# Kernel tuning notes

Measured on AMD Instinct MI355X. Metric: run time of the kernel, lower is better.

The kernel has to match this reference:

```python
import jax, jax.numpy as jnp
import numpy as np

B, NORB, N_UP, N_DN, HIDDEN = 1024, 128, 32, 32, 4096


def setup_inputs() -> dict:
    rng = np.random.default_rng(0)
    # Build valid occupancy configs: exactly N_UP up-electrons (bit 0) and
    # N_DN down-electrons (bit 1) per sample. Encoding: 0=empty,1=up,2=dn,3=updn.
    up_order = np.argsort(rng.random((B, NORB)), axis=1)
    dn_order = np.argsort(rng.random((B, NORB)), axis=1)
    up_bit = np.zeros((B, NORB), np.int32)
    dn_bit = np.zeros((B, NORB), np.int32)
    np.put_along_axis(up_bit, up_order[:, :N_UP], 1, axis=1)
    np.put_along_axis(dn_bit, dn_order[:, :N_DN], 1, axis=1)
    x = jnp.asarray(up_bit + 2 * dn_bit, dtype=jnp.int32)

    key = jax.random.key(0)
    k1, k2, k3 = jax.random.split(key, 3)
    orbitals = jax.random.normal(k1, (NORB, N_UP), jnp.float32)
    W1 = jax.random.normal(k2, (4 * NORB, HIDDEN), jnp.float32) / np.sqrt(4 * NORB)
    b1 = jnp.zeros((HIDDEN,), jnp.float32)
    W2 = jax.random.normal(k3, (HIDDEN, NORB * N_UP), jnp.float32) / np.sqrt(HIDDEN)
    b2 = jnp.zeros((NORB * N_UP,), jnp.float32)
    return {"x": x, "orbitals": orbitals, "W1": W1, "b1": b1, "W2": W2, "b2": b2}


def _occupancies_to_electrons(x, n_up, n_dn):
    # Per-spin sorted positions of occupied orbitals. Stable argsort on the
    # inverted mask keeps occupied sites first, in ascending orbital order.
    up_mask = (x & 1) == 1
    dn_mask = (x & 2) == 2
    y_up = jnp.argsort(jnp.where(up_mask, 0, 1), axis=-1, stable=True)[:, :n_up]
    y_dn = jnp.argsort(jnp.where(dn_mask, 0, 1), axis=-1, stable=True)[:, :n_dn]
    return y_up, y_dn


def reference(x, orbitals, W1, b1, W2, b2):
    Bsz, norb = x.shape
    n_up = orbitals.shape[1]

    # correction_fun: MLP on one-hot config -> [B, norb, n_up]
    h = jax.nn.one_hot(x, 4, dtype=W1.dtype).reshape(Bsz, -1)  # [B, 4*norb]
    h = jax.nn.relu(h @ W1 + b1)                               # [B, hidden]
    corrections = (h @ W2 + b2).reshape(Bsz, norb, n_up)       # [B, norb, n_up]

    y_up, y_dn = _occupancies_to_electrons(x, n_up, n_up)
    y_up = y_up[..., None]  # [B, n_up, 1]
    y_dn = y_dn[..., None]

    # gather orbital rows + correction rows per electron (spin-symmetric orbitals)
    phi_up = jnp.take_along_axis(orbitals[None], y_up, axis=1)  # [B, n_up, n_up]
    phi_dn = jnp.take_along_axis(orbitals[None], y_dn, axis=1)
    d_up = jnp.take_along_axis(corrections, y_up, axis=1)
    d_dn = jnp.take_along_axis(corrections, y_dn, axis=1)

    s_up, log_det_up = jnp.linalg.slogdet(phi_up + d_up)
    s_dn, log_det_dn = jnp.linalg.slogdet(phi_dn + d_dn)
    return log_det_up + log_det_dn + jnp.log(s_up * s_dn + 0j)  # complex [B]
```

## Files before the change

### kernel.cpp

```cpp
#include <hip/hip_runtime.h>
#include <cmath>

#define B_SZ  1024
#define NORB  128
#define NUP   32
#define HID   4096
#define NCORR (NORB * NUP)
#define K1    (4 * NORB)

typedef short    bf16x8 __attribute__((ext_vector_type(8)));
typedef _Float16 f16x8  __attribute__((ext_vector_type(8)));
typedef float    f32x4  __attribute__((ext_vector_type(4)));

__device__ __forceinline__ unsigned short f2bf_rne(float f) {
    unsigned int u = __float_as_uint(f);
    u += 0x7FFFu + ((u >> 16) & 1u);
    return (unsigned short)(u >> 16);
}

__global__ __launch_bounds__(256) void k_pack(const float* __restrict__ W1,
                                              unsigned short* __restrict__ W1ph,
                                              unsigned short* __restrict__ W1pl,
                                              const float* __restrict__ W2,
                                              _Float16* __restrict__ Bh16,
                                              _Float16* __restrict__ Bl16) {
    __shared__ float tile[64][33];
    int bid = blockIdx.x;
    int t = threadIdx.x;

    int isW2 = (bid >= 1024);
    int i = isW2 ? bid - 1024 : bid;
    int n0 = (i & 127) * 32;
    int k0 = (i >> 7) * 64;
    const float* W = isW2 ? W2 : W1;

    int rl = t >> 3, c4 = (t & 7) * 4;
#pragma unroll
    for (int q = 0; q < 2; ++q) {
        int kl = rl + 32 * q;
        float4 v = *(const float4*)(W + (size_t)(k0 + kl) * 4096 + n0 + c4);
        tile[kl][c4 + 0] = v.x; tile[kl][c4 + 1] = v.y;
        tile[kl][c4 + 2] = v.z; tile[kl][c4 + 3] = v.w;
    }
    __syncthreads();

    int nl = t & 31, kg = t >> 5;
    int nt = (n0 + nl) >> 4;
    int kt = (k0 >> 5) + (kg >> 2);
    int lane_o = (kg & 3) * 16 + (nl & 15);

    if (isW2) {
        size_t o = (((size_t)nt * 128 + kt) * 64 + lane_o) * 8;
        f16x8 hi8, lo8;
#pragma unroll
        for (int j = 0; j < 8; ++j) {
            float v = tile[kg * 8 + j][nl];
            _Float16 hi = (_Float16)v;
            hi8[j] = hi;
            lo8[j] = (_Float16)((v - (float)hi) * 2048.0f);
        }
        *(f16x8*)(Bh16 + o) = hi8;
        *(f16x8*)(Bl16 + o) = lo8;
    } else {
        size_t o = (((size_t)nt * 16 + kt) * 64 + lane_o) * 8;
        unsigned short hi8[8], lo8[8];
#pragma unroll
        for (int j = 0; j < 8; ++j) {
            float v = tile[kg * 8 + j][nl];
            unsigned short hi = f2bf_rne(v);
            float fhi = __uint_as_float((unsigned int)hi << 16);
            hi8[j] = hi;
            lo8[j] = f2bf_rne(v - fhi);
        }
        *(bf16x8*)(W1ph + o) = *(bf16x8*)hi8;
        *(bf16x8*)(W1pl + o) = *(bf16x8*)lo8;
    }
}

__global__ __launch_bounds__(256, 2) void k_hidden3(const int* __restrict__ x,
                                                    const unsigned short* __restrict__ Bph,
                                                    const unsigned short* __restrict__ Bpl,
                                                    const float* __restrict__ b1,
                                                    _Float16* __restrict__ h16) {
    __shared__ unsigned int sxp[64][8];
    __shared__ unsigned short BF[2][4][4][512];
    __shared__ float Ht[64][132];

    int n0 = blockIdx.x * 128;
    int m0 = blockIdx.y * 64;
    int t = threadIdx.x;
    int w = t >> 6, lane = t & 63;
    int lm = lane & 15, kq = lane >> 4;
    int wn = w * 32;

#pragma unroll
    for (int i = 0; i < 2; ++i) {
        int id = t + 256 * i;
        int row = id >> 3, d = id & 7;
        const int* src = x + (size_t)(m0 + row) * NORB + d * 16;
        unsigned int dw = 0;
#pragma unroll
        for (int b = 0; b < 16; ++b) dw |= ((unsigned int)(src[b] & 3)) << (2 * b);
        sxp[row][d] = dw;
    }

    int nt0 = (n0 + wn) >> 4;
    const unsigned short* bh0 = Bph + (size_t)nt0 * (16 * 512) + (size_t)lane * 8;
    const unsigned short* bh1 = Bph + (size_t)(nt0 + 1) * (16 * 512) + (size_t)lane * 8;
    const unsigned short* bl0 = Bpl + (size_t)nt0 * (16 * 512) + (size_t)lane * 8;
    const unsigned short* bl1 = Bpl + (size_t)(nt0 + 1) * (16 * 512) + (size_t)lane * 8;

    f32x4 acc[4][2] = {};

    bf16x8 r0 = *(const bf16x8*)(bh0);
    bf16x8 r1 = *(const bf16x8*)(bh1);
    bf16x8 r2 = *(const bf16x8*)(bl0);
    bf16x8 r3 = *(const bf16x8*)(bl1);
    bf16x8 r4 = *(const bf16x8*)(bh0 + 512);
    bf16x8 r5 = *(const bf16x8*)(bh1 + 512);
    bf16x8 r6 = *(const bf16x8*)(bl0 + 512);
    bf16x8 r7 = *(const bf16x8*)(bl1 + 512);

    __syncthreads();

    for (int p = 0; p < 8; ++p) {
        if (p) __syncthreads();

        *(bf16x8*)&BF[0][w][0][lane * 8] = r0;
        *(bf16x8*)&BF[0][w][1][lane * 8] = r1;
        *(bf16x8*)&BF[0][w][2][lane * 8] = r2;
        *(bf16x8*)&BF[0][w][3][lane * 8] = r3;
        *(bf16x8*)&BF[1][w][0][lane * 8] = r4;
        *(bf16x8*)&BF[1][w][1][lane * 8] = r5;
        *(bf16x8*)&BF[1][w][2][lane * 8] = r6;
        *(bf16x8*)&BF[1][w][3][lane * 8] = r7;
        __syncthreads();

        int kn = (p + 1 < 8) ? p + 1 : 7;
        r0 = *(const bf16x8*)(bh0 + (2 * kn) * 512);
        r1 = *(const bf16x8*)(bh1 + (2 * kn) * 512);
        r2 = *(const bf16x8*)(bl0 + (2 * kn) * 512);
        r3 = *(const bf16x8*)(bl1 + (2 * kn) * 512);
        r4 = *(const bf16x8*)(bh0 + (2 * kn + 1) * 512);
        r5 = *(const bf16x8*)(bh1 + (2 * kn + 1) * 512);
        r6 = *(const bf16x8*)(bl0 + (2 * kn + 1) * 512);
        r7 = *(const bf16x8*)(bl1 + (2 * kn + 1) * 512);
        __builtin_amdgcn_sched_barrier(0);

#pragma unroll
        for (int s = 0; s < 2; ++s) {
            int kt = 2 * p + s;
            int i0 = kt * 8 + kq * 2;
            int dwIdx = i0 >> 4;
            int sh = (i0 & 15) * 2;
            bf16x8 af[4];
#pragma unroll
            for (int fm = 0; fm < 4; ++fm) {
                unsigned int dw = sxp[fm * 16 + lm][dwIdx];
                unsigned int c01 = (dw >> sh) & 0xFu;
                union { bf16x8 v; unsigned long long u[2]; } a;
                a.u[0] = 0x3F80ULL << ((c01 & 3u) * 16);
                a.u[1] = 0x3F80ULL << ((c01 >> 2) * 16);
                af[fm] = a.v;
            }

            bf16x8 b0h = *(const bf16x8*)&BF[s][w][0][lane * 8];
            bf16x8 b1h = *(const bf16x8*)&BF[s][w][1][lane * 8];
            bf16x8 b0l = *(const bf16x8*)&BF[s][w][2][lane * 8];
            bf16x8 b1l = *(const bf16x8*)&BF[s][w][3][lane * 8];

#pragma unroll
            for (int fm = 0; fm < 4; ++fm) {
                acc[fm][0] = __builtin_amdgcn_mfma_f32_16x16x32_bf16(af[fm], b0h, acc[fm][0], 0, 0, 0);
                acc[fm][0] = __builtin_amdgcn_mfma_f32_16x16x32_bf16(af[fm], b0l, acc[fm][0], 0, 0, 0);
                acc[fm][1] = __builtin_amdgcn_mfma_f32_16x16x32_bf16(af[fm], b1h, acc[fm][1], 0, 0, 0);
                acc[fm][1] = __builtin_amdgcn_mfma_f32_16x16x32_bf16(af[fm], b1l, acc[fm][1], 0, 0, 0);
            }
        }
    }

    __syncthreads();
#pragma unroll
    for (int fm = 0; fm < 4; ++fm)
#pragma unroll
        for (int fn = 0; fn < 2; ++fn) {
            int n = wn + fn * 16 + lm;
            float bv = b1[n0 + n];
#pragma unroll
            for (int r = 0; r < 4; ++r)
                Ht[fm * 16 + kq * 4 + r][n] = fmaxf(acc[fm][fn][r] + bv, 0.f);
        }
    __syncthreads();

    size_t mt0 = (size_t)(m0 >> 4), kt0 = (size_t)(n0 >> 5);
#pragma unroll
    for (int fi = 0; fi < 4; ++fi) {
        int f = w * 4 + fi;
        int mt = f >> 2, ktn = f & 3;
        int m = mt * 16 + lm;
        int kn = ktn * 32 + kq * 8;
        float4 v0 = *(const float4*)&Ht[m][kn];
        float4 v1 = *(const float4*)&Ht[m][kn + 4];
        float vv[8] = {v0.x, v0.y, v0.z, v0.w, v1.x, v1.y, v1.z, v1.w};
        f16x8 o16;
#pragma unroll
        for (int j = 0; j < 8; ++j) o16[j] = (_Float16)vv[j];
        size_t o = (((mt0 + mt) * 128 + (kt0 + ktn)) * 64 + lane) * 8;
        *(f16x8*)(h16 + o) = o16;
    }
}

__global__ __launch_bounds__(256) void k_hidden_f32(const int* __restrict__ x,
                                                    const float* __restrict__ W1,
                                                    const float* __restrict__ b1,
                                                    float* __restrict__ h) {
    int b = blockIdx.x, tid = threadIdx.x;
    __shared__ int sx[NORB];
    if (tid < NORB) sx[tid] = x[b * NORB + tid];
    __syncthreads();
    float acc[16];
#pragma unroll
    for (int u = 0; u < 16; ++u) acc[u] = b1[tid + 256 * u];
    for (int i = 0; i < NORB; ++i) {
        const float* row = W1 + (size_t)(4 * i + sx[i]) * HID;
#pragma unroll
        for (int u = 0; u < 16; ++u) acc[u] += row[tid + 256 * u];
    }
    float* hb = h + (size_t)b * HID;
#pragma unroll
    for (int u = 0; u < 16; ++u) hb[tid + 256 * u] = fmaxf(acc[u], 0.f);
}

__global__ __launch_bounds__(256, 2) void k_gemm7(const _Float16* __restrict__ Ap,
                                                  const _Float16* __restrict__ Bph,
                                                  const _Float16* __restrict__ Bpl,
                                                  const float* __restrict__ bias,
                                                  float* __restrict__ C) {
    __shared__ _Float16 AF[2][2][4][512];

    int n0 = blockIdx.x * 128;
    int m0 = blockIdx.y * 64;
    int t = threadIdx.x;
    int w = t >> 6, lane = t & 63;
    int lm = lane & 15, kq = lane >> 4;
    int wn = w * 32;

    int mt0 = m0 >> 4;
    int nt0 = (n0 + wn) >> 4;

    const _Float16* ag  = Ap  + (size_t)(mt0 + w) * 65536 + (size_t)lane * 8;
    const _Float16* bh0 = Bph + (size_t)nt0 * 65536 + (size_t)lane * 8;
    const _Float16* bh1 = Bph + (size_t)(nt0 + 1) * 65536 + (size_t)lane * 8;
    const _Float16* bl0 = Bpl + (size_t)nt0 * 65536 + (size_t)lane * 8;
    const _Float16* bl1 = Bpl + (size_t)(nt0 + 1) * 65536 + (size_t)lane * 8;

    f32x4 accH[4][2] = {}, accL[4][2] = {};

    f16x8 r0 = *(const f16x8*)(ag);
    f16x8 r1 = *(const f16x8*)(ag + 512);
    f16x8 B0h0 = *(const f16x8*)(bh0);
    f16x8 B0h1 = *(const f16x8*)(bh1);
    f16x8 B0l0 = *(const f16x8*)(bl0);
    f16x8 B0l1 = *(const f16x8*)(bl1);
    f16x8 B1h0 = *(const f16x8*)(bh0 + 512);
    f16x8 B1h1 = *(const f16x8*)(bh1 + 512);
    f16x8 B1l0 = *(const f16x8*)(bl0 + 512);
    f16x8 B1l1 = *(const f16x8*)(bl1 + 512);

    for (int ktp = 0; ktp < 64; ++ktp) {
        int buf = ktp & 1;
        *(f16x8*)&AF[buf][0][w][lane * 8] = r0;
        *(f16x8*)&AF[buf][1][w][lane * 8] = r1;
        __syncthreads();

        int kn = (ktp + 1 < 64) ? ktp + 1 : 63;
        size_t o0 = (size_t)(2 * kn) * 512, o1 = o0 + 512;
        f16x8 nr0 = *(const f16x8*)(ag + o0);
        f16x8 nr1 = *(const f16x8*)(ag + o1);
        f16x8 nB0h0 = *(const f16x8*)(bh0 + o0);
        f16x8 nB0h1 = *(const f16x8*)(bh1 + o0);
        f16x8 nB0l0 = *(const f16x8*)(bl0 + o0);
        f16x8 nB0l1 = *(const f16x8*)(bl1 + o0);
        f16x8 nB1h0 = *(const f16x8*)(bh0 + o1);
        f16x8 nB1h1 = *(const f16x8*)(bh1 + o1);
        f16x8 nB1l0 = *(const f16x8*)(bl0 + o1);
        f16x8 nB1l1 = *(const f16x8*)(bl1 + o1);
        __builtin_amdgcn_sched_barrier(0);

        f16x8 a0[4], a1[4];
#pragma unroll
        for (int fm = 0; fm < 4; ++fm) {
            a0[fm] = *(const f16x8*)&AF[buf][0][fm][lane * 8];
            a1[fm] = *(const f16x8*)&AF[buf][1][fm][lane * 8];
        }

#pragma unroll
        for (int fm = 0; fm < 4; ++fm) {
            accH[fm][0] = __builtin_amdgcn_mfma_f32_16x16x32_f16(a0[fm], B0h0, accH[fm][0], 0, 0, 0);
            accL[fm][0] = __builtin_amdgcn_mfma_f32_16x16x32_f16(a0[fm], B0l0, accL[fm][0], 0, 0, 0);
            accH[fm][1] = __builtin_amdgcn_mfma_f32_16x16x32_f16(a0[fm], B0h1, accH[fm][1], 0, 0, 0);
            accL[fm][1] = __builtin_amdgcn_mfma_f32_16x16x32_f16(a0[fm], B0l1, accL[fm][1], 0, 0, 0);
        }
#pragma unroll
        for (int fm = 0; fm < 4; ++fm) {
            accH[fm][0] = __builtin_amdgcn_mfma_f32_16x16x32_f16(a1[fm], B1h0, accH[fm][0], 0, 0, 0);
            accL[fm][0] = __builtin_amdgcn_mfma_f32_16x16x32_f16(a1[fm], B1l0, accL[fm][0], 0, 0, 0);
            accH[fm][1] = __builtin_amdgcn_mfma_f32_16x16x32_f16(a1[fm], B1h1, accH[fm][1], 0, 0, 0);
            accL[fm][1] = __builtin_amdgcn_mfma_f32_16x16x32_f16(a1[fm], B1l1, accL[fm][1], 0, 0, 0);
        }

        r0 = nr0; r1 = nr1;
        B0h0 = nB0h0; B0h1 = nB0h1; B0l0 = nB0l0; B0l1 = nB0l1;
        B1h0 = nB1h0; B1h1 = nB1h1; B1l0 = nB1l0; B1l1 = nB1l1;
    }

    const float ls = 1.0f / 2048.0f;
#pragma unroll
    for (int fm = 0; fm < 4; ++fm)
#pragma unroll
        for (int fn = 0; fn < 2; ++fn) {
            int n = n0 + wn + fn * 16 + lm;
            float bv = bias[n];
#pragma unroll
            for (int r = 0; r < 4; ++r) {
                int m = m0 + fm * 16 + kq * 4 + r;
                C[(size_t)m * NCORR + n] = accH[fm][fn][r] + ls * accL[fm][fn][r] + bv;
            }
        }
}

#define BM 64
#define BN 64
#define BK 32
__global__ __launch_bounds__(256) void k_gemm(const float* __restrict__ A,
                                              const float* __restrict__ Bm,
                                              const float* __restrict__ bias,
                                              float* __restrict__ C) {
    __shared__ float As[BK][68];
    __shared__ float Bs[BK][BN];
    int n0 = blockIdx.x * BN, m0 = blockIdx.y * BM;
    int tid = threadIdx.x;
    int tm = tid >> 4, tn = tid & 15;
    int am = tid >> 3, ak = (tid & 7) * 4;
    int bk = tid >> 4, bn = (tid & 15) * 4;
    float acc[4][4] = {};
    for (int k0 = 0; k0 < HID; k0 += BK) {
#pragma unroll
        for (int s = 0; s < 2; ++s) {
            int m = am + 32 * s;
            float4 v = *(const float4*)(A + (size_t)(m0 + m) * HID + k0 + ak);
            As[ak + 0][m] = v.x; As[ak + 1][m] = v.y;
            As[ak + 2][m] = v.z; As[ak + 3][m] = v.w;
        }
#pragma unroll
        for (int s = 0; s < 2; ++s) {
            int k = bk + 16 * s;
            float4 v = *(const float4*)(Bm + (size_t)(k0 + k) * NCORR + n0 + bn);
            *(float4*)&Bs[k][bn] = v;
        }
        __syncthreads();
#pragma unroll
        for (int kk = 0; kk < BK; ++kk) {
            float4 a = *(const float4*)&As[kk][tm * 4];
            float4 bv = *(const float4*)&Bs[kk][tn * 4];
            float av[4] = {a.x, a.y, a.z, a.w};
            float bb[4] = {bv.x, bv.y, bv.z, bv.w};
#pragma unroll
            for (int i = 0; i < 4; ++i)
#pragma unroll
                for (int j = 0; j < 4; ++j) acc[i][j] += av[i] * bb[j];
        }
        __syncthreads();
    }
#pragma unroll
    for (int i = 0; i < 4; ++i) {
        int m = m0 + tm * 4 + i;
        float4 o;
        o.x = acc[i][0] + bias[n0 + tn * 4 + 0];
        o.y = acc[i][1] + bias[n0 + tn * 4 + 1];
        o.z = acc[i][2] + bias[n0 + tn * 4 + 2];
        o.w = acc[i][3] + bias[n0 + tn * 4 + 3];
        *(float4*)(C + (size_t)m * NCORR + n0 + tn * 4) = o;
    }
}

__global__ __launch_bounds__(128) void k_det(const int* __restrict__ x,
                                             const float* __restrict__ orbitals,
                                             const float* __restrict__ corr,
                                             float* __restrict__ out,
                                             int imag_off) {
    int b = blockIdx.x, tid = threadIdx.x;
    __shared__ int sx[NORB];
    __shared__ int yup[NUP], ydn[NUP];
    __shared__ float M[2][NUP][NUP + 1];
    __shared__ float rlog[2];
    __shared__ int rneg[2];

    sx[tid] = x[b * NORB + tid];
    __syncthreads();

    int occ = sx[tid];
    if (occ & 1) {
        int r = 0;
        for (int i = 0; i < tid; ++i) r += sx[i] & 1;
        yup[r] = tid;
    }
    if (occ & 2) {
        int r = 0;
        for (int i = 0; i < tid; ++i) r += (sx[i] >> 1) & 1;
        ydn[r] = tid;
    }
    __syncthreads();

    const float* cb = corr + (size_t)b * NCORR;
    for (int idx = tid; idx < 2 * NUP * NUP; idx += 128) {
        int s = idx >> 10;
        int i = (idx >> 5) & 31;
        int j = idx & 31;
        int r = s ? ydn[i] : yup[i];
        M[s][i][j] = orbitals[r * NUP + j] + cb[r * NUP + j];
    }
    __syncthreads();

    int wv = tid >> 6, lane = tid & 63;
    float (*Mm)[NUP + 1] = M[wv];
    float logdet = 0.f;
    int neg = 0;

    for (int k = 0; k < NUP; ++k) {
        float v = (lane >= k && lane < NUP) ? fabsf(Mm[lane][k]) : -1.f;
        int pi = lane;
#pragma unroll
        for (int off = 32; off > 0; off >>= 1) {
            float v2 = __shfl_down(v, off);
            int p2 = __shfl_down(pi, off);
            if (v2 > v) { v = v2; pi = p2; }
        }
        int p = __shfl(pi, 0);

        if (p != k) {
            if (lane < NUP) {
                float t1 = Mm[k][lane];
                Mm[k][lane] = Mm[p][lane];
                Mm[p][lane] = t1;
            }
            neg ^= 1;
        }
        __syncthreads();

        float pv = Mm[k][k];
        logdet += logf(fabsf(pv));
        if (pv < 0.f) neg ^= 1;

        int row = k + 1 + (lane & 31);
        int half = lane >> 5;
        if (row < NUP) {
            float f = Mm[row][k] / pv;
            for (int j = k + 1 + half; j < NUP; j += 2)
                Mm[row][j] -= f * Mm[k][j];
        }
        __syncthreads();
    }

    if (lane == 0) { rlog[wv] = logdet; rneg[wv] = neg; }
    __syncthreads();
    if (tid == 0) {
        out[b] = rlog[0] + rlog[1];
        if (imag_off > 0)
            out[imag_off + b] =
                (rneg[0] ^ rneg[1]) ? 3.14159265358979323846f : 0.f;
    }
}

extern "C" void kernel_launch(void* const* d_in, const int* in_sizes, int n_in,
                              void* d_out, int out_size, void* d_ws, size_t ws_size,
                              hipStream_t stream) {
    const int*   x        = (const int*)d_in[0];
    const float* orbitals = (const float*)d_in[1];
    const float* W1       = (const float*)d_in[2];
    const float* b1       = (const float*)d_in[3];
    const float* W2       = (const float*)d_in[4];
    const float* b2       = (const float*)d_in[5];
    float* out = (float*)d_out;
    int imag_off = (out_size == 2 * B_SZ) ? B_SZ : 0;

    const size_t need = (size_t)96 * 1024 * 1024;
    if (ws_size >= need) {
        _Float16* h16  = (_Float16*)d_ws;
        _Float16* Bh16 = h16 + (size_t)B_SZ * HID;
        _Float16* Bl16 = Bh16 + (size_t)HID * NCORR;
        float*    corr = (float*)(Bl16 + (size_t)HID * NCORR);

        unsigned short* W1ph = (unsigned short*)corr;
        unsigned short* W1pl = W1ph + (size_t)K1 * HID;

        k_pack<<<1024 + 8192, 256, 0, stream>>>(W1, W1ph, W1pl,
                                                W2, Bh16, Bl16);

        k_hidden3<<<dim3(HID / 128, B_SZ / 64), 256, 0, stream>>>(x, W1ph, W1pl, b1, h16);

        dim3 g2(NCORR / 128, B_SZ / 64);
        k_gemm7<<<g2, 256, 0, stream>>>(h16, Bh16, Bl16, b2, corr);

        k_det<<<B_SZ, 128, 0, stream>>>(x, orbitals, corr, out, imag_off);
    } else {
        float* h    = (float*)d_ws;
        float* corr = h + (size_t)B_SZ * HID;
        k_hidden_f32<<<B_SZ, 256, 0, stream>>>(x, W1, b1, h);
        dim3 g2(NCORR / BN, B_SZ / BM);
        k_gemm<<<g2, 256, 0, stream>>>(h, W2, b2, corr);
        k_det<<<B_SZ, 128, 0, stream>>>(x, orbitals, corr, out, imag_off);
    }
}
```

Baseline: 239.4 us.

## Swizzle GEMM block order for cache locality and use ballot for electron ranks

The GEMM launch becomes a 1D grid with a block-index remap. Consecutive blocks are spread across the 8 XCDs, and each XCD gets a 4x16 group of output tiles, so A and B tiles are reused in that XCD's L2. The determinant kernel replaces the serial per-thread prefix count over shared memory with wave ballots and popcounts to rank occupied orbitals. The remap assumes round-robin dispatch of blocks to XCDs and a fixed grid size of 512.

```diff
diff --git a/kernel.cpp b/kernel.cpp
--- a/kernel.cpp
+++ b/kernel.cpp
@@ -238,8 +238,12 @@
                                                   float* __restrict__ C) {
     __shared__ _Float16 AF[2][2][4][512];
 
-    int n0 = blockIdx.x * 128;
-    int m0 = blockIdx.y * 64;
+    int bid = blockIdx.x;
+    int lb = (bid & 7) * 64 + (bid >> 3);
+    int local = lb & 63;
+    int n0 = ((lb >> 6) * 4 + (local >> 4)) * 128;
+    int m0 = (local & 15) * 64;
+
     int t = threadIdx.x;
     int w = t >> 6, lane = t & 63;
     int lm = lane & 15, kq = lane >> 4;
@@ -390,26 +394,24 @@
                                              float* __restrict__ out,
                                              int imag_off) {
     int b = blockIdx.x, tid = threadIdx.x;
-    __shared__ int sx[NORB];
     __shared__ int yup[NUP], ydn[NUP];
+    __shared__ int cnt0[2];
     __shared__ float M[2][NUP][NUP + 1];
     __shared__ float rlog[2];
     __shared__ int rneg[2];
 
-    sx[tid] = x[b * NORB + tid];
-    __syncthreads();
-
-    int occ = sx[tid];
-    if (occ & 1) {
-        int r = 0;
-        for (int i = 0; i < tid; ++i) r += sx[i] & 1;
-        yup[r] = tid;
-    }
-    if (occ & 2) {
-        int r = 0;
-        for (int i = 0; i < tid; ++i) r += (sx[i] >> 1) & 1;
-        ydn[r] = tid;
-    }
+    int occ = x[b * NORB + tid];
+    int lane0 = tid & 63;
+    unsigned long long mup = __ballot(occ & 1);
+    unsigned long long mdn = __ballot((occ >> 1) & 1);
+    if (tid == 0) { cnt0[0] = __popcll(mup); cnt0[1] = __popcll(mdn); }
+    __syncthreads();
+
+    unsigned long long below = (1ull << lane0) - 1ull;
+    int bu = (tid >= 64) ? cnt0[0] : 0;
+    int bd = (tid >= 64) ? cnt0[1] : 0;
+    if (occ & 1) yup[bu + __popcll(mup & below)] = tid;
+    if (occ & 2) ydn[bd + __popcll(mdn & below)] = tid;
     __syncthreads();
 
     const float* cb = corr + (size_t)b * NCORR;
@@ -499,8 +501,7 @@
 
         k_hidden3<<<dim3(HID / 128, B_SZ / 64), 256, 0, stream>>>(x, W1ph, W1pl, b1, h16);
 
-        dim3 g2(NCORR / 128, B_SZ / 64);
-        k_gemm7<<<g2, 256, 0, stream>>>(h16, Bh16, Bl16, b2, corr);
+        k_gemm7<<<512, 256, 0, stream>>>(h16, Bh16, Bl16, b2, corr);
 
         k_det<<<B_SZ, 128, 0, stream>>>(x, orbitals, corr, out, imag_off);
     } else {
```

After: 235.9 us. Within noise of the previous version (-1.5%).
